# Kernel tuning notes

Hardware: AMD Instinct MI355X
Metric: run time of the kernel (lower is better)

The kernel has to match this reference:

```python
import jax, jax.numpy as jnp
import numpy as np

N = 50000      # nodes
E = 800000     # edges (avg degree 16)
IN = 128       # input feature dim
HID = 32       # per-head hidden dim
OUT = 64       # per-head output dim
H = 2          # heads per layer
NEG = 0.2      # leaky relu negative slope


def setup_inputs() -> dict:
    key = jax.random.key(0)
    ks = jax.random.split(key, 16)
    x = jax.random.normal(ks[0], (N, IN), dtype=jnp.float32)
    src = jax.random.randint(ks[1], (E,), 0, N)
    dst = jax.random.randint(ks[2], (E,), 0, N)

    def lin(k, fin, fout):
        return jax.random.normal(k, (fin, fout), dtype=jnp.float32) * (1.0 / np.sqrt(fin))

    def attn(k, h, d):
        return jax.random.normal(k, (h, d), dtype=jnp.float32) * 0.1

    # layer 0: IN -> H*HID, layer 1: H*HID -> H*HID, layer 2 (output): H*HID -> H*OUT
    W0, al0, ar0, b0 = lin(ks[3], IN, H * HID), attn(ks[4], H, HID), attn(ks[5], H, HID), jnp.zeros((H * HID,), jnp.float32)
    W1, al1, ar1, b1 = lin(ks[6], H * HID, H * HID), attn(ks[7], H, HID), attn(ks[8], H, HID), jnp.zeros((H * HID,), jnp.float32)
    W2, al2, ar2, b2 = lin(ks[9], H * HID, H * OUT), attn(ks[10], H, OUT), attn(ks[11], H, OUT), jnp.zeros((H * OUT,), jnp.float32)
    return {"x": x, "src": src, "dst": dst,
            "W0": W0, "al0": al0, "ar0": ar0, "b0": b0,
            "W1": W1, "al1": al1, "ar1": ar1, "b1": b1,
            "W2": W2, "al2": al2, "ar2": ar2, "b2": b2}


def gat_conv(x, src, dst, W, al, ar, b, heads, out_dim, apply_relu):
    # feat: [N, H, D]
    feat = (x @ W).reshape(-1, heads, out_dim)
    el = jnp.einsum('nhd,hd->nh', feat, al)   # [N, H]
    er = jnp.einsum('nhd,hd->nh', feat, ar)   # [N, H]
    # per-edge attention logits, leaky-relu
    e = jax.nn.leaky_relu(el[src] + er[dst], NEG)          # [E, H]
    # edge softmax over incoming edges of each dst node (numerically stable)
    m = jax.ops.segment_max(e, dst, num_segments=N)        # [N, H]
    m = jnp.where(jnp.isfinite(m), m, 0.0)                 # nodes w/o in-edges
    ex = jnp.exp(e - m[dst])                               # [E, H]
    s = jax.ops.segment_sum(ex, dst, num_segments=N)       # [N, H]
    alpha = ex / s[dst]                                    # [E, H]
    # weighted aggregate of source features into dst nodes
    rst = jax.ops.segment_sum(feat[src] * alpha[:, :, None], dst, num_segments=N)  # [N, H, D]
    rst = rst + b.reshape(1, heads, out_dim)
    if apply_relu:
        rst = jax.nn.relu(rst)
    return rst


def reference(x, src, dst, W0, al0, ar0, b0, W1, al1, ar1, b1, W2, al2, ar2, b2):
    h = gat_conv(x, src, dst, W0, al0, ar0, b0, H, HID, True).reshape(N, H * HID)   # flatten(1)
    h = gat_conv(h, src, dst, W1, al1, ar1, b1, H, HID, True).reshape(N, H * HID)   # flatten(1)
    logits = gat_conv(h, src, dst, W2, al2, ar2, b2, H, OUT, False).mean(axis=1)    # mean over heads -> [N, OUT]
    return logits
```

## Files before the change

kernel.cpp:

```cpp
#include <hip/hip_runtime.h>
#include <hip/hip_bf16.h>
#include <hip/hip_fp16.h>

#define NNODES 50000
#define NEG_SLOPE 0.2f
#define BKT_SHIFT 8
#define NBKT ((NNODES + 255) >> 8)
#define PEPT 8

typedef _Float16 half8 __attribute__((ext_vector_type(8)));
typedef float v4f __attribute__((ext_vector_type(4)));

__device__ __forceinline__ int rfl(int v) { return __builtin_amdgcn_readfirstlane(v); }

__device__ __forceinline__ void pack_one(const float* W, _Float16* Wp, int K, int C, int tid) {
    int KC = K / 32;
    int l = tid & 63;
    int kc = (tid >> 6) % KC;
    int t = tid / (KC * 64);
    int cc = l & 15, q = l >> 4;
    half8 b;
#pragma unroll
    for (int j = 0; j < 8; j++)
        b[j] = (_Float16)W[(size_t)(kc * 32 + q * 8 + j) * C + t * 16 + cc];
    *(half8*)(Wp + (size_t)tid * 8) = b;
}

__global__ void bucket_hist_pack(const int* __restrict__ dst, int* __restrict__ bhist, int E,
                                 const float* __restrict__ W0, _Float16* __restrict__ Wp0,
                                 const float* __restrict__ W1, _Float16* __restrict__ Wp1,
                                 const float* __restrict__ W2, _Float16* __restrict__ Wp2) {
    if (blockIdx.x >= 512) {
        int tid = (blockIdx.x - 512) * 256 + threadIdx.x;
        const int t0 = 4 * 4 * 64, t1 = 4 * 2 * 64, t2 = 8 * 2 * 64;
        if (tid < t0) pack_one(W0, Wp0, 128, 64, tid);
        else if (tid < t0 + t1) pack_one(W1, Wp1, 64, 64, tid - t0);
        else if (tid < t0 + t1 + t2) pack_one(W2, Wp2, 64, 128, tid - t0 - t1);
        return;
    }
    __shared__ int lh[NBKT];
    for (int i = threadIdx.x; i < NBKT; i += 256) lh[i] = 0;
    __syncthreads();
    const int4* d4 = (const int4*)dst;
    int E4 = E >> 2;
    for (int i = blockIdx.x * 256 + threadIdx.x; i < E4; i += 512 * 256) {
        int4 d = d4[i];
        atomicAdd(&lh[d.x >> BKT_SHIFT], 1);
        atomicAdd(&lh[d.y >> BKT_SHIFT], 1);
        atomicAdd(&lh[d.z >> BKT_SHIFT], 1);
        atomicAdd(&lh[d.w >> BKT_SHIFT], 1);
    }
    if (blockIdx.x == 0 && threadIdx.x < (E & 3))
        atomicAdd(&lh[dst[(E4 << 2) + threadIdx.x] >> BKT_SHIFT], 1);
    __syncthreads();
    for (int i = threadIdx.x; i < NBKT; i += 256)
        if (lh[i]) atomicAdd(&bhist[i], lh[i]);
}

__global__ void scan_buckets(const int* __restrict__ bhist, int* __restrict__ bbase,
                             int* __restrict__ bcursor) {
    __shared__ int buf[256];
    int t = threadIdx.x;
    int v = (t < NBKT) ? bhist[t] : 0;
    buf[t] = v;
    __syncthreads();
    for (int off = 1; off < 256; off <<= 1) {
        int x = (t >= off) ? buf[t - off] : 0;
        __syncthreads();
        buf[t] += x;
        __syncthreads();
    }
    if (t < NBKT) { int e = buf[t] - v; bbase[t] = e; bcursor[t * 16] = e; }
}

__global__ __launch_bounds__(1024) void partition_edges(
    const int* __restrict__ src, const int* __restrict__ dst,
    int* __restrict__ bcursor, int2* __restrict__ ebuf, int E) {
    __shared__ int hist[NBKT];
    __shared__ int gbase[NBKT];
    int t = threadIdx.x;
    for (int i = t; i < NBKT; i += 1024) hist[i] = 0;
    __syncthreads();
    int base = blockIdx.x * 1024 * PEPT;
    int sreg[PEPT], dreg[PEPT], rreg[PEPT], breg[PEPT];
#pragma unroll
    for (int k = 0; k < PEPT; k++) {
        int i = base + k * 1024 + t;
        if (i < E) {
            sreg[k] = src[i];
            dreg[k] = dst[i];
            breg[k] = dreg[k] >> BKT_SHIFT;
            rreg[k] = atomicAdd(&hist[breg[k]], 1);
        } else {
            breg[k] = -1;
        }
    }
    __syncthreads();
    for (int i = t; i < NBKT; i += 1024)
        if (hist[i]) gbase[i] = atomicAdd(&bcursor[i * 16], hist[i]);
    __syncthreads();
#pragma unroll
    for (int k = 0; k < PEPT; k++) {
        if (breg[k] >= 0)
            ebuf[(size_t)(gbase[breg[k]] + rreg[k])] = make_int2(sreg[k], dreg[k]);
    }
}

__global__ __launch_bounds__(256) void local_sort(const int2* __restrict__ ebuf,
                                                  const int* __restrict__ bbase,
                                                  int* __restrict__ rowptr,
                                                  int* __restrict__ csrc, int N, int E) {
    __shared__ int lcnt[256], lrow[256], ws[4];
    int b = blockIdx.x;
    int d0 = b << BKT_SHIFT;
    int t = threadIdx.x;
    int base = bbase[b];
    int endE = (b + 1 < NBKT) ? bbase[b + 1] : E;
    lcnt[t] = 0;
    __syncthreads();
    for (int i = base + t; i < endE; i += 256)
        atomicAdd(&lcnt[ebuf[i].y - d0], 1);
    __syncthreads();
    int v = lcnt[t];
    int lane = t & 63;
    int x = v;
#pragma unroll
    for (int m = 1; m < 64; m <<= 1) {
        int y = __shfl_up(x, m, 64);
        if (lane >= m) x += y;
    }
    if (lane == 63) ws[t >> 6] = x;
    __syncthreads();
    int w = t >> 6, waveoff = 0;
#pragma unroll
    for (int k = 0; k < 4; k++) if (k < w) waveoff += ws[k];
    int excl = base + waveoff + x - v;
    lrow[t] = excl;
    int d = d0 + t;
    if (d < N) rowptr[d] = excl;
    if (d == N) rowptr[N] = excl;
    lcnt[t] = 0;
    __syncthreads();
    for (int i = base + t; i < endE; i += 256) {
        int2 e = ebuf[i];
        int ld = e.y - d0;
        int p = lrow[ld] + atomicAdd(&lcnt[ld], 1);
        csrc[p] = e.x;
    }
}

template <int K, int C, bool INTERLEAVE, bool AFP32>
__global__ __launch_bounds__(256) void gemm_mfma(
    const void* __restrict__ Ahi_, const void* __restrict__ Alo_,
    const _Float16* __restrict__ Wp,
    const float* __restrict__ AL, const float* __restrict__ AR,
    void* __restrict__ featout, float2* __restrict__ el2, float2* __restrict__ er2,
    int N) {
    constexpr int KC = K / 32;
    constexpr int NT = C / 16;
    int wave = threadIdx.x >> 6, lane = threadIdx.x & 63;
    int mtile = blockIdx.x * 4 + wave;
    if (mtile * 16 >= N) return;
    int m0 = mtile * 16;
    int c = lane & 15, q = lane >> 4;

    v4f acc[NT];
#pragma unroll
    for (int t = 0; t < NT; t++) acc[t] = (v4f){0.f, 0.f, 0.f, 0.f};

    const size_t arow = (size_t)(m0 + c) * K + q * 8;
#pragma unroll
    for (int kc = 0; kc < KC; kc++) {
        half8 ah, av;
        if constexpr (AFP32) {
            const float* xr = (const float*)Ahi_ + arow + kc * 32;
            float4 f0 = *(const float4*)xr;
            float4 f1 = *(const float4*)(xr + 4);
            float fv[8] = {f0.x, f0.y, f0.z, f0.w, f1.x, f1.y, f1.z, f1.w};
#pragma unroll
            for (int j = 0; j < 8; j++) {
                ah[j] = (_Float16)fv[j];
                av[j] = (_Float16)(fv[j] - (float)ah[j]);
            }
        } else {
            ah = *(const half8*)((const _Float16*)Ahi_ + arow + kc * 32);
            av = *(const half8*)((const _Float16*)Alo_ + arow + kc * 32);
        }
#pragma unroll
        for (int t = 0; t < NT; t++) {
            half8 b = *(const half8*)(Wp + ((size_t)(t * KC + kc) * 64 + lane) * 8);
            acc[t] = __builtin_amdgcn_mfma_f32_16x16x32_f16(ah, b, acc[t], 0, 0, 0);
            acc[t] = __builtin_amdgcn_mfma_f32_16x16x32_f16(av, b, acc[t], 0, 0, 0);
        }
    }

    if (!INTERLEAVE) {
        _Float16* f16 = (_Float16*)featout;
#pragma unroll
        for (int t = 0; t < NT; t++)
#pragma unroll
            for (int r = 0; r < 4; r++) {
                int row = m0 + q * 4 + r;
                f16[(size_t)row * C + t * 16 + c] = (_Float16)acc[t][r];
            }
    } else {
        __half2* f2 = (__half2*)featout;
#pragma unroll
        for (int t = 0; t < NT / 2; t++)
#pragma unroll
            for (int r = 0; r < 4; r++) {
                int row = m0 + q * 4 + r;
                f2[(size_t)row * (C / 2) + t * 16 + c] =
                    __floats2half2_rn(acc[t][r], acc[t + NT / 2][r]);
            }
    }

    float alv[NT], arv[NT];
#pragma unroll
    for (int t = 0; t < NT; t++) { alv[t] = AL[t * 16 + c]; arv[t] = AR[t * 16 + c]; }
#pragma unroll
    for (int r = 0; r < 4; r++) {
        float l0 = 0.f, l1 = 0.f, r0 = 0.f, r1 = 0.f;
#pragma unroll
        for (int t = 0; t < NT; t++) {
            float v = acc[t][r];
            if (t < NT / 2) { l0 = fmaf(v, alv[t], l0); r0 = fmaf(v, arv[t], r0); }
            else            { l1 = fmaf(v, alv[t], l1); r1 = fmaf(v, arv[t], r1); }
        }
#pragma unroll
        for (int m = 1; m < 16; m <<= 1) {
            l0 += __shfl_xor(l0, m, 64);
            l1 += __shfl_xor(l1, m, 64);
            r0 += __shfl_xor(r0, m, 64);
            r1 += __shfl_xor(r1, m, 64);
        }
        if (c == 0) {
            int row = m0 + q * 4 + r;
            el2[row] = make_float2(l0, l1);
            er2[row] = make_float2(r0, r1);
        }
    }
}

__global__ __launch_bounds__(256) void aggregate32(
    const int* __restrict__ rowptr, const int* __restrict__ csrc,
    const float2* __restrict__ el2, const float2* __restrict__ er2,
    const _Float16* __restrict__ feat16, const float* __restrict__ b,
    _Float16* __restrict__ ahi, _Float16* __restrict__ alo, int N) {
    __shared__ int2 stA[4][64], stB[4][64];
    int wave = threadIdx.x >> 6, lane = threadIdx.x & 63, h = lane >> 5;
    int n = rfl(blockIdx.x * 4 + wave);
    if (n >= N) return;
    float bl = b[lane];
    int beg = rfl(rowptr[n]), end = rfl(rowptr[n + 1]);
    float2 rr = er2[n];
    const int2* stH = h ? stB[wave] : stA[wave];
    float s = 0.f, acc = 0.f;
    for (int base = beg; base < end; base += 64) {
        int idx = base + lane;
        int sv = 0; float wxv = 0.f, wyv = 0.f;
        if (idx < end) {
            sv = csrc[idx];
            float2 l = el2[sv];
            float t0 = l.x + rr.x; t0 = t0 > 0.f ? t0 : NEG_SLOPE * t0;
            float t1 = l.y + rr.y; t1 = t1 > 0.f ? t1 : NEG_SLOPE * t1;
            wxv = __expf(t0); wyv = __expf(t1);
        }
        stA[wave][lane] = make_int2(sv, __float_as_int(wxv));
        stB[wave][lane] = make_int2(sv, __float_as_int(wyv));
        int cnt = min(64, end - base);
        int j = 0;
        for (; j + 7 < cnt; j += 8) {
            int4 e01 = *(const int4*)(stH + j);
            int4 e23 = *(const int4*)(stH + j + 2);
            int4 e45 = *(const int4*)(stH + j + 4);
            int4 e67 = *(const int4*)(stH + j + 6);
            float f0 = (float)feat16[(size_t)e01.x * 64 + lane];
            float f1 = (float)feat16[(size_t)e01.z * 64 + lane];
            float f2 = (float)feat16[(size_t)e23.x * 64 + lane];
            float f3 = (float)feat16[(size_t)e23.z * 64 + lane];
            float f4 = (float)feat16[(size_t)e45.x * 64 + lane];
            float f5 = (float)feat16[(size_t)e45.z * 64 + lane];
            float f6 = (float)feat16[(size_t)e67.x * 64 + lane];
            float f7 = (float)feat16[(size_t)e67.z * 64 + lane];
            float w0 = __int_as_float(e01.y), w1 = __int_as_float(e01.w);
            float w2 = __int_as_float(e23.y), w3 = __int_as_float(e23.w);
            float w4 = __int_as_float(e45.y), w5 = __int_as_float(e45.w);
            float w6 = __int_as_float(e67.y), w7 = __int_as_float(e67.w);
            s += ((w0 + w1) + (w2 + w3)) + ((w4 + w5) + (w6 + w7));
            acc = fmaf(w0, f0, acc);
            acc = fmaf(w1, f1, acc);
            acc = fmaf(w2, f2, acc);
            acc = fmaf(w3, f3, acc);
            acc = fmaf(w4, f4, acc);
            acc = fmaf(w5, f5, acc);
            acc = fmaf(w6, f6, acc);
            acc = fmaf(w7, f7, acc);
        }
        for (; j < cnt; j++) {
            int2 e = stH[j];
            float w0 = __int_as_float(e.y);
            float f0 = (float)feat16[(size_t)e.x * 64 + lane];
            s += w0;
            acc = fmaf(w0, f0, acc);
        }
    }
    float v = (s > 0.f) ? acc / s : 0.f;
    v = fmaxf(v + bl, 0.f);
    _Float16 hv = (_Float16)v;
    ahi[(size_t)n * 64 + lane] = hv;
    alo[(size_t)n * 64 + lane] = (_Float16)(v - (float)hv);
}

__global__ __launch_bounds__(256) void aggregate64_mean(
    const int* __restrict__ rowptr, const int* __restrict__ csrc,
    const float2* __restrict__ el2, const float2* __restrict__ er2,
    const __half2* __restrict__ feat2, const float* __restrict__ b,
    float* __restrict__ out, int N) {
    __shared__ int4 st[4][64];
    int wave = threadIdx.x >> 6, lane = threadIdx.x & 63;
    int n = rfl(blockIdx.x * 4 + wave);
    if (n >= N) return;
    float b0 = b[lane], b1 = b[64 + lane];
    int beg = rfl(rowptr[n]), end = rfl(rowptr[n + 1]);
    float2 rr = er2[n];
    float s0 = 0.f, s1 = 0.f, a0 = 0.f, a1 = 0.f;
    for (int base = beg; base < end; base += 64) {
        int idx = base + lane;
        int sv = 0; float wxv = 0.f, wyv = 0.f;
        if (idx < end) {
            sv = csrc[idx];
            float2 l = el2[sv];
            float t0 = l.x + rr.x; t0 = t0 > 0.f ? t0 : NEG_SLOPE * t0;
            float t1 = l.y + rr.y; t1 = t1 > 0.f ? t1 : NEG_SLOPE * t1;
            wxv = __expf(t0); wyv = __expf(t1);
        }
        st[wave][lane] = make_int4(sv, __float_as_int(wxv), __float_as_int(wyv), 0);
        int cnt = min(64, end - base);
        int j = 0;
        for (; j + 7 < cnt; j += 8) {
            float2 fv[8]; float wxs[8], wys[8];
#pragma unroll
            for (int u = 0; u < 8; u++) {
                int4 e = st[wave][j + u];
                wxs[u] = __int_as_float(e.y);
                wys[u] = __int_as_float(e.z);
                fv[u] = __half22float2(feat2[(size_t)e.x * 64 + lane]);
            }
#pragma unroll
            for (int u = 0; u < 8; u++) {
                s0 += wxs[u]; s1 += wys[u];
                a0 = fmaf(wxs[u], fv[u].x, a0);
                a1 = fmaf(wys[u], fv[u].y, a1);
            }
        }
        for (; j < cnt; j++) {
            int4 e = st[wave][j];
            float wx0 = __int_as_float(e.y), wy0 = __int_as_float(e.z);
            float2 f0 = __half22float2(feat2[(size_t)e.x * 64 + lane]);
            s0 += wx0; s1 += wy0;
            a0 = fmaf(wx0, f0.x, a0); a1 = fmaf(wy0, f0.y, a1);
        }
    }
    float v0 = (s0 > 0.f) ? a0 / s0 : 0.f;
    float v1 = (s1 > 0.f) ? a1 / s1 : 0.f;
    out[(size_t)n * 64 + lane] = 0.5f * ((v0 + b0) + (v1 + b1));
}


extern "C" void kernel_launch(void* const* d_in, const int* in_sizes, int n_in,
                              void* d_out, int out_size, void* d_ws, size_t ws_size,
                              hipStream_t stream) {
    const float* x   = (const float*)d_in[0];
    const int*   src = (const int*)d_in[1];
    const int*   dst = (const int*)d_in[2];
    const float* W0  = (const float*)d_in[3];
    const float* al0 = (const float*)d_in[4];
    const float* ar0 = (const float*)d_in[5];
    const float* b0  = (const float*)d_in[6];
    const float* W1  = (const float*)d_in[7];
    const float* al1 = (const float*)d_in[8];
    const float* ar1 = (const float*)d_in[9];
    const float* b1  = (const float*)d_in[10];
    const float* W2  = (const float*)d_in[11];
    const float* al2 = (const float*)d_in[12];
    const float* ar2 = (const float*)d_in[13];
    const float* b2  = (const float*)d_in[14];
    float* out = (float*)d_out;

    const int N = NNODES;
    const int E = in_sizes[1];

    char* p = (char*)d_ws;
    auto alloc = [&](size_t bytes) {
        void* r = (void*)p;
        p += (bytes + 255) & ~(size_t)255;
        return r;
    };
    int*    bhist    = (int*)alloc((size_t)NBKT * 4);
    int*    bbase    = (int*)alloc((size_t)NBKT * 4);
    int*    bcursor  = (int*)alloc((size_t)NBKT * 16 * 4);
    int*    rowptr   = (int*)alloc((size_t)(N + 1) * 4);
    int2*   ebuf     = (int2*)alloc((size_t)E * 8);
    int*    csrc     = (int*)alloc((size_t)E * 4);
    float2* el2      = (float2*)alloc((size_t)N * 8);
    float2* er2      = (float2*)alloc((size_t)N * 8);
    _Float16* ahi    = (_Float16*)alloc((size_t)N * 64 * 2);
    _Float16* alo    = (_Float16*)alloc((size_t)N * 64 * 2);
    void*   featbuf  = alloc((size_t)N * 64 * 4);
    _Float16* Wp0    = (_Float16*)alloc(4 * 4 * 64 * 8 * 2);
    _Float16* Wp1    = (_Float16*)alloc(4 * 2 * 64 * 8 * 2);
    _Float16* Wp2    = (_Float16*)alloc(8 * 2 * 64 * 8 * 2);
    _Float16* feat16 = (_Float16*)featbuf;
    __half2*  feat2  = (__half2*)featbuf;

    hipMemsetAsync(bhist, 0, (size_t)NBKT * 4, stream);
    bucket_hist_pack<<<522, 256, 0, stream>>>(dst, bhist, E, W0, Wp0, W1, Wp1, W2, Wp2);
    scan_buckets<<<1, 256, 0, stream>>>(bhist, bbase, bcursor);
    int pb = (E + 1024 * PEPT - 1) / (1024 * PEPT);
    partition_edges<<<pb, 1024, 0, stream>>>(src, dst, bcursor, ebuf, E);
    local_sort<<<NBKT, 256, 0, stream>>>(ebuf, bbase, rowptr, csrc, N, E);

    int nb4 = (N + 3) / 4;
    int gb = (N / 16 + 3) / 4;

    gemm_mfma<128, 64, false, true><<<gb, 256, 0, stream>>>(x, nullptr, Wp0, al0, ar0, featbuf, el2, er2, N);
    aggregate32<<<nb4, 256, 0, stream>>>(rowptr, csrc, el2, er2, feat16, b0, ahi, alo, N);

    gemm_mfma<64, 64, false, false><<<gb, 256, 0, stream>>>(ahi, alo, Wp1, al1, ar1, featbuf, el2, er2, N);
    aggregate32<<<nb4, 256, 0, stream>>>(rowptr, csrc, el2, er2, feat16, b1, ahi, alo, N);

    gemm_mfma<64, 128, true, false><<<gb, 256, 0, stream>>>(ahi, alo, Wp2, al2, ar2, featbuf, el2, er2, N);
    aggregate64_mean<<<nb4, 256, 0, stream>>>(rowptr, csrc, el2, er2, feat2, b2, out, N);
}
```

Before: 257.4 us.

## Fuse all GAT stages into one persistent cooperative kernel with grid syncs

Replaces the sequence of separate launches (histogram/pack, scan, partition, local sort, three gemm and three aggregate kernels) with one cooperative persistent kernel. Each stage becomes a device phase with grid-stride loops, separated by grid.sync(), and all phases share one shared-memory union. The edge partition now walks fixed 8192-edge chunks and keeps per-edge ranks in shared memory instead of registers. This targets per-launch overhead and the memset. In exchange it adds grid-wide barrier costs, limits the grid to at most 1024 blocks, and raises shared-memory and register pressure, which may lower occupancy in the gather-heavy aggregate phases.

New measurement: 943.5 us. 267% more time.

```diff
diff --git a/kernel.cpp b/kernel.cpp
--- a/kernel.cpp
+++ b/kernel.cpp
@@ -1,17 +1,46 @@
 #include <hip/hip_runtime.h>
 #include <hip/hip_bf16.h>
 #include <hip/hip_fp16.h>
+#include <hip/hip_cooperative_groups.h>
+
+namespace cg = cooperative_groups;
 
 #define NNODES 50000
 #define NEG_SLOPE 0.2f
 #define BKT_SHIFT 8
 #define NBKT ((NNODES + 255) >> 8)
-#define PEPT 8
+#define CHUNK 8192
 
 typedef _Float16 half8 __attribute__((ext_vector_type(8)));
 typedef float v4f __attribute__((ext_vector_type(4)));
 
 __device__ __forceinline__ int rfl(int v) { return __builtin_amdgcn_readfirstlane(v); }
+
+struct PartSM { int hist[NBKT]; int gbase[NBKT]; unsigned short rank[CHUNK]; };
+struct LsortSM { int lcnt[256]; int lrow[256]; int ws[4]; };
+struct Agg32SM { int2 stA[4][64]; int2 stB[4][64]; };
+union SMem {
+    int lh[NBKT];
+    int scanbuf[256];
+    PartSM part;
+    LsortSM lsort;
+    Agg32SM agg32;
+    int4 st64[4][64];
+};
+
+struct GArgs {
+    const float* x; const int* src; const int* dst;
+    const float *W0, *al0, *ar0, *b0;
+    const float *W1, *al1, *ar1, *b1;
+    const float *W2, *al2, *ar2, *b2;
+    float* out; int E;
+    int *bhist, *bbase, *bcursor, *rowptr;
+    int2* ebuf; int* csrc;
+    float2 *el2, *er2;
+    _Float16 *ahi, *alo;
+    void* featbuf;
+    _Float16 *Wp0, *Wp1, *Wp2;
+};
 
 __device__ __forceinline__ void pack_one(const float* W, _Float16* Wp, int K, int C, int tid) {
     int KC = K / 32;
@@ -26,368 +55,350 @@
     *(half8*)(Wp + (size_t)tid * 8) = b;
 }
 
-__global__ void bucket_hist_pack(const int* __restrict__ dst, int* __restrict__ bhist, int E,
-                                 const float* __restrict__ W0, _Float16* __restrict__ Wp0,
-                                 const float* __restrict__ W1, _Float16* __restrict__ Wp1,
-                                 const float* __restrict__ W2, _Float16* __restrict__ Wp2) {
-    if (blockIdx.x >= 512) {
-        int tid = (blockIdx.x - 512) * 256 + threadIdx.x;
-        const int t0 = 4 * 4 * 64, t1 = 4 * 2 * 64, t2 = 8 * 2 * 64;
-        if (tid < t0) pack_one(W0, Wp0, 128, 64, tid);
-        else if (tid < t0 + t1) pack_one(W1, Wp1, 64, 64, tid - t0);
-        else if (tid < t0 + t1 + t2) pack_one(W2, Wp2, 64, 128, tid - t0 - t1);
-        return;
-    }
-    __shared__ int lh[NBKT];
-    for (int i = threadIdx.x; i < NBKT; i += 256) lh[i] = 0;
-    __syncthreads();
-    const int4* d4 = (const int4*)dst;
-    int E4 = E >> 2;
-    for (int i = blockIdx.x * 256 + threadIdx.x; i < E4; i += 512 * 256) {
-        int4 d = d4[i];
-        atomicAdd(&lh[d.x >> BKT_SHIFT], 1);
-        atomicAdd(&lh[d.y >> BKT_SHIFT], 1);
-        atomicAdd(&lh[d.z >> BKT_SHIFT], 1);
-        atomicAdd(&lh[d.w >> BKT_SHIFT], 1);
-    }
-    if (blockIdx.x == 0 && threadIdx.x < (E & 3))
-        atomicAdd(&lh[dst[(E4 << 2) + threadIdx.x] >> BKT_SHIFT], 1);
-    __syncthreads();
-    for (int i = threadIdx.x; i < NBKT; i += 256)
-        if (lh[i]) atomicAdd(&bhist[i], lh[i]);
-}
-
-__global__ void scan_buckets(const int* __restrict__ bhist, int* __restrict__ bbase,
-                             int* __restrict__ bcursor) {
-    __shared__ int buf[256];
-    int t = threadIdx.x;
-    int v = (t < NBKT) ? bhist[t] : 0;
-    buf[t] = v;
-    __syncthreads();
-    for (int off = 1; off < 256; off <<= 1) {
-        int x = (t >= off) ? buf[t - off] : 0;
-        __syncthreads();
-        buf[t] += x;
-        __syncthreads();
-    }
-    if (t < NBKT) { int e = buf[t] - v; bbase[t] = e; bcursor[t * 16] = e; }
-}
-
-__global__ __launch_bounds__(1024) void partition_edges(
-    const int* __restrict__ src, const int* __restrict__ dst,
-    int* __restrict__ bcursor, int2* __restrict__ ebuf, int E) {
-    __shared__ int hist[NBKT];
-    __shared__ int gbase[NBKT];
-    int t = threadIdx.x;
-    for (int i = t; i < NBKT; i += 1024) hist[i] = 0;
-    __syncthreads();
-    int base = blockIdx.x * 1024 * PEPT;
-    int sreg[PEPT], dreg[PEPT], rreg[PEPT], breg[PEPT];
-#pragma unroll
-    for (int k = 0; k < PEPT; k++) {
-        int i = base + k * 1024 + t;
-        if (i < E) {
-            sreg[k] = src[i];
-            dreg[k] = dst[i];
-            breg[k] = dreg[k] >> BKT_SHIFT;
-            rreg[k] = atomicAdd(&hist[breg[k]], 1);
-        } else {
-            breg[k] = -1;
-        }
-    }
-    __syncthreads();
-    for (int i = t; i < NBKT; i += 1024)
-        if (hist[i]) gbase[i] = atomicAdd(&bcursor[i * 16], hist[i]);
-    __syncthreads();
-#pragma unroll
-    for (int k = 0; k < PEPT; k++) {
-        if (breg[k] >= 0)
-            ebuf[(size_t)(gbase[breg[k]] + rreg[k])] = make_int2(sreg[k], dreg[k]);
-    }
-}
-
-__global__ __launch_bounds__(256) void local_sort(const int2* __restrict__ ebuf,
-                                                  const int* __restrict__ bbase,
-                                                  int* __restrict__ rowptr,
-                                                  int* __restrict__ csrc, int N, int E) {
-    __shared__ int lcnt[256], lrow[256], ws[4];
-    int b = blockIdx.x;
-    int d0 = b << BKT_SHIFT;
-    int t = threadIdx.x;
-    int base = bbase[b];
-    int endE = (b + 1 < NBKT) ? bbase[b + 1] : E;
-    lcnt[t] = 0;
-    __syncthreads();
-    for (int i = base + t; i < endE; i += 256)
-        atomicAdd(&lcnt[ebuf[i].y - d0], 1);
-    __syncthreads();
-    int v = lcnt[t];
-    int lane = t & 63;
-    int x = v;
-#pragma unroll
-    for (int m = 1; m < 64; m <<= 1) {
-        int y = __shfl_up(x, m, 64);
-        if (lane >= m) x += y;
-    }
-    if (lane == 63) ws[t >> 6] = x;
-    __syncthreads();
-    int w = t >> 6, waveoff = 0;
-#pragma unroll
-    for (int k = 0; k < 4; k++) if (k < w) waveoff += ws[k];
-    int excl = base + waveoff + x - v;
-    lrow[t] = excl;
-    int d = d0 + t;
-    if (d < N) rowptr[d] = excl;
-    if (d == N) rowptr[N] = excl;
-    lcnt[t] = 0;
-    __syncthreads();
-    for (int i = base + t; i < endE; i += 256) {
-        int2 e = ebuf[i];
-        int ld = e.y - d0;
-        int p = lrow[ld] + atomicAdd(&lcnt[ld], 1);
-        csrc[p] = e.x;
-    }
-}
-
 template <int K, int C, bool INTERLEAVE, bool AFP32>
-__global__ __launch_bounds__(256) void gemm_mfma(
-    const void* __restrict__ Ahi_, const void* __restrict__ Alo_,
-    const _Float16* __restrict__ Wp,
-    const float* __restrict__ AL, const float* __restrict__ AR,
-    void* __restrict__ featout, float2* __restrict__ el2, float2* __restrict__ er2,
-    int N) {
+__device__ void gemm_phase(const GArgs& a, const void* Ahi_, const void* Alo_,
+                           const _Float16* Wp, const float* AL, const float* AR,
+                           int gridBlocks) {
     constexpr int KC = K / 32;
     constexpr int NT = C / 16;
     int wave = threadIdx.x >> 6, lane = threadIdx.x & 63;
-    int mtile = blockIdx.x * 4 + wave;
-    if (mtile * 16 >= N) return;
-    int m0 = mtile * 16;
     int c = lane & 15, q = lane >> 4;
-
-    v4f acc[NT];
-#pragma unroll
-    for (int t = 0; t < NT; t++) acc[t] = (v4f){0.f, 0.f, 0.f, 0.f};
-
-    const size_t arow = (size_t)(m0 + c) * K + q * 8;
-#pragma unroll
-    for (int kc = 0; kc < KC; kc++) {
-        half8 ah, av;
-        if constexpr (AFP32) {
-            const float* xr = (const float*)Ahi_ + arow + kc * 32;
-            float4 f0 = *(const float4*)xr;
-            float4 f1 = *(const float4*)(xr + 4);
-            float fv[8] = {f0.x, f0.y, f0.z, f0.w, f1.x, f1.y, f1.z, f1.w};
-#pragma unroll
-            for (int j = 0; j < 8; j++) {
-                ah[j] = (_Float16)fv[j];
-                av[j] = (_Float16)(fv[j] - (float)ah[j]);
-            }
+    const int MT = NNODES / 16;
+    for (int mtile = blockIdx.x * 4 + wave; mtile < MT; mtile += gridBlocks * 4) {
+        int m0 = mtile * 16;
+        v4f acc[NT];
+#pragma unroll
+        for (int t = 0; t < NT; t++) acc[t] = (v4f){0.f, 0.f, 0.f, 0.f};
+        const size_t arow = (size_t)(m0 + c) * K + q * 8;
+#pragma unroll
+        for (int kc = 0; kc < KC; kc++) {
+            half8 ah, av;
+            if constexpr (AFP32) {
+                const float* xr = (const float*)Ahi_ + arow + kc * 32;
+                float4 f0 = *(const float4*)xr;
+                float4 f1 = *(const float4*)(xr + 4);
+                float fv[8] = {f0.x, f0.y, f0.z, f0.w, f1.x, f1.y, f1.z, f1.w};
+#pragma unroll
+                for (int j = 0; j < 8; j++) {
+                    ah[j] = (_Float16)fv[j];
+                    av[j] = (_Float16)(fv[j] - (float)ah[j]);
+                }
+            } else {
+                ah = *(const half8*)((const _Float16*)Ahi_ + arow + kc * 32);
+                av = *(const half8*)((const _Float16*)Alo_ + arow + kc * 32);
+            }
+#pragma unroll
+            for (int t = 0; t < NT; t++) {
+                half8 b = *(const half8*)(Wp + ((size_t)(t * KC + kc) * 64 + lane) * 8);
+                acc[t] = __builtin_amdgcn_mfma_f32_16x16x32_f16(ah, b, acc[t], 0, 0, 0);
+                acc[t] = __builtin_amdgcn_mfma_f32_16x16x32_f16(av, b, acc[t], 0, 0, 0);
+            }
+        }
+        if (!INTERLEAVE) {
+            _Float16* f16 = (_Float16*)a.featbuf;
+#pragma unroll
+            for (int t = 0; t < NT; t++)
+#pragma unroll
+                for (int r = 0; r < 4; r++) {
+                    int row = m0 + q * 4 + r;
+                    f16[(size_t)row * C + t * 16 + c] = (_Float16)acc[t][r];
+                }
         } else {
-            ah = *(const half8*)((const _Float16*)Ahi_ + arow + kc * 32);
-            av = *(const half8*)((const _Float16*)Alo_ + arow + kc * 32);
-        }
-#pragma unroll
-        for (int t = 0; t < NT; t++) {
-            half8 b = *(const half8*)(Wp + ((size_t)(t * KC + kc) * 64 + lane) * 8);
-            acc[t] = __builtin_amdgcn_mfma_f32_16x16x32_f16(ah, b, acc[t], 0, 0, 0);
-            acc[t] = __builtin_amdgcn_mfma_f32_16x16x32_f16(av, b, acc[t], 0, 0, 0);
-        }
-    }
-
-    if (!INTERLEAVE) {
-        _Float16* f16 = (_Float16*)featout;
-#pragma unroll
-        for (int t = 0; t < NT; t++)
-#pragma unroll
-            for (int r = 0; r < 4; r++) {
+            __half2* f2 = (__half2*)a.featbuf;
+#pragma unroll
+            for (int t = 0; t < NT / 2; t++)
+#pragma unroll
+                for (int r = 0; r < 4; r++) {
+                    int row = m0 + q * 4 + r;
+                    f2[(size_t)row * (C / 2) + t * 16 + c] =
+                        __floats2half2_rn(acc[t][r], acc[t + NT / 2][r]);
+                }
+        }
+        float alv[NT], arv[NT];
+#pragma unroll
+        for (int t = 0; t < NT; t++) { alv[t] = AL[t * 16 + c]; arv[t] = AR[t * 16 + c]; }
+#pragma unroll
+        for (int r = 0; r < 4; r++) {
+            float l0 = 0.f, l1 = 0.f, r0 = 0.f, r1 = 0.f;
+#pragma unroll
+            for (int t = 0; t < NT; t++) {
+                float v = acc[t][r];
+                if (t < NT / 2) { l0 = fmaf(v, alv[t], l0); r0 = fmaf(v, arv[t], r0); }
+                else            { l1 = fmaf(v, alv[t], l1); r1 = fmaf(v, arv[t], r1); }
+            }
+#pragma unroll
+            for (int m = 1; m < 16; m <<= 1) {
+                l0 += __shfl_xor(l0, m, 64);
+                l1 += __shfl_xor(l1, m, 64);
+                r0 += __shfl_xor(r0, m, 64);
+                r1 += __shfl_xor(r1, m, 64);
+            }
+            if (c == 0) {
                 int row = m0 + q * 4 + r;
-                f16[(size_t)row * C + t * 16 + c] = (_Float16)acc[t][r];
-            }
-    } else {
-        __half2* f2 = (__half2*)featout;
-#pragma unroll
-        for (int t = 0; t < NT / 2; t++)
-#pragma unroll
-            for (int r = 0; r < 4; r++) {
-                int row = m0 + q * 4 + r;
-                f2[(size_t)row * (C / 2) + t * 16 + c] =
-                    __floats2half2_rn(acc[t][r], acc[t + NT / 2][r]);
-            }
-    }
-
-    float alv[NT], arv[NT];
-#pragma unroll
-    for (int t = 0; t < NT; t++) { alv[t] = AL[t * 16 + c]; arv[t] = AR[t * 16 + c]; }
-#pragma unroll
-    for (int r = 0; r < 4; r++) {
-        float l0 = 0.f, l1 = 0.f, r0 = 0.f, r1 = 0.f;
-#pragma unroll
-        for (int t = 0; t < NT; t++) {
-            float v = acc[t][r];
-            if (t < NT / 2) { l0 = fmaf(v, alv[t], l0); r0 = fmaf(v, arv[t], r0); }
-            else            { l1 = fmaf(v, alv[t], l1); r1 = fmaf(v, arv[t], r1); }
-        }
-#pragma unroll
-        for (int m = 1; m < 16; m <<= 1) {
-            l0 += __shfl_xor(l0, m, 64);
-            l1 += __shfl_xor(l1, m, 64);
-            r0 += __shfl_xor(r0, m, 64);
-            r1 += __shfl_xor(r1, m, 64);
-        }
-        if (c == 0) {
-            int row = m0 + q * 4 + r;
-            el2[row] = make_float2(l0, l1);
-            er2[row] = make_float2(r0, r1);
-        }
-    }
-}
-
-__global__ __launch_bounds__(256) void aggregate32(
-    const int* __restrict__ rowptr, const int* __restrict__ csrc,
-    const float2* __restrict__ el2, const float2* __restrict__ er2,
-    const _Float16* __restrict__ feat16, const float* __restrict__ b,
-    _Float16* __restrict__ ahi, _Float16* __restrict__ alo, int N) {
-    __shared__ int2 stA[4][64], stB[4][64];
+                a.el2[row] = make_float2(l0, l1);
+                a.er2[row] = make_float2(r0, r1);
+            }
+        }
+    }
+}
+
+__device__ void agg32_phase(const GArgs& a, SMem& sm, const float* b,
+                            int gridBlocks) {
     int wave = threadIdx.x >> 6, lane = threadIdx.x & 63, h = lane >> 5;
-    int n = rfl(blockIdx.x * 4 + wave);
-    if (n >= N) return;
     float bl = b[lane];
-    int beg = rfl(rowptr[n]), end = rfl(rowptr[n + 1]);
-    float2 rr = er2[n];
-    const int2* stH = h ? stB[wave] : stA[wave];
-    float s = 0.f, acc = 0.f;
-    for (int base = beg; base < end; base += 64) {
-        int idx = base + lane;
-        int sv = 0; float wxv = 0.f, wyv = 0.f;
-        if (idx < end) {
-            sv = csrc[idx];
-            float2 l = el2[sv];
-            float t0 = l.x + rr.x; t0 = t0 > 0.f ? t0 : NEG_SLOPE * t0;
-            float t1 = l.y + rr.y; t1 = t1 > 0.f ? t1 : NEG_SLOPE * t1;
-            wxv = __expf(t0); wyv = __expf(t1);
-        }
-        stA[wave][lane] = make_int2(sv, __float_as_int(wxv));
-        stB[wave][lane] = make_int2(sv, __float_as_int(wyv));
-        int cnt = min(64, end - base);
-        int j = 0;
-        for (; j + 7 < cnt; j += 8) {
-            int4 e01 = *(const int4*)(stH + j);
-            int4 e23 = *(const int4*)(stH + j + 2);
-            int4 e45 = *(const int4*)(stH + j + 4);
-            int4 e67 = *(const int4*)(stH + j + 6);
-            float f0 = (float)feat16[(size_t)e01.x * 64 + lane];
-            float f1 = (float)feat16[(size_t)e01.z * 64 + lane];
-            float f2 = (float)feat16[(size_t)e23.x * 64 + lane];
-            float f3 = (float)feat16[(size_t)e23.z * 64 + lane];
-            float f4 = (float)feat16[(size_t)e45.x * 64 + lane];
-            float f5 = (float)feat16[(size_t)e45.z * 64 + lane];
-            float f6 = (float)feat16[(size_t)e67.x * 64 + lane];
-            float f7 = (float)feat16[(size_t)e67.z * 64 + lane];
-            float w0 = __int_as_float(e01.y), w1 = __int_as_float(e01.w);
-            float w2 = __int_as_float(e23.y), w3 = __int_as_float(e23.w);
-            float w4 = __int_as_float(e45.y), w5 = __int_as_float(e45.w);
-            float w6 = __int_as_float(e67.y), w7 = __int_as_float(e67.w);
-            s += ((w0 + w1) + (w2 + w3)) + ((w4 + w5) + (w6 + w7));
-            acc = fmaf(w0, f0, acc);
-            acc = fmaf(w1, f1, acc);
-            acc = fmaf(w2, f2, acc);
-            acc = fmaf(w3, f3, acc);
-            acc = fmaf(w4, f4, acc);
-            acc = fmaf(w5, f5, acc);
-            acc = fmaf(w6, f6, acc);
-            acc = fmaf(w7, f7, acc);
-        }
-        for (; j < cnt; j++) {
-            int2 e = stH[j];
-            float w0 = __int_as_float(e.y);
-            float f0 = (float)feat16[(size_t)e.x * 64 + lane];
-            s += w0;
-            acc = fmaf(w0, f0, acc);
-        }
-    }
-    float v = (s > 0.f) ? acc / s : 0.f;
-    v = fmaxf(v + bl, 0.f);
-    _Float16 hv = (_Float16)v;
-    ahi[(size_t)n * 64 + lane] = hv;
-    alo[(size_t)n * 64 + lane] = (_Float16)(v - (float)hv);
-}
-
-__global__ __launch_bounds__(256) void aggregate64_mean(
-    const int* __restrict__ rowptr, const int* __restrict__ csrc,
-    const float2* __restrict__ el2, const float2* __restrict__ er2,
-    const __half2* __restrict__ feat2, const float* __restrict__ b,
-    float* __restrict__ out, int N) {
-    __shared__ int4 st[4][64];
+    const _Float16* feat16 = (const _Float16*)a.featbuf;
+    const int2* stH = h ? sm.agg32.stB[wave] : sm.agg32.stA[wave];
+    for (int n0 = blockIdx.x * 4 + wave; n0 < NNODES; n0 += gridBlocks * 4) {
+        int n = rfl(n0);
+        int beg = rfl(a.rowptr[n]), end = rfl(a.rowptr[n + 1]);
+        float2 rr = a.er2[n];
+        float s = 0.f, acc = 0.f;
+        for (int base = beg; base < end; base += 64) {
+            int idx = base + lane;
+            int sv = 0; float wxv = 0.f, wyv = 0.f;
+            if (idx < end) {
+                sv = a.csrc[idx];
+                float2 l = a.el2[sv];
+                float t0 = l.x + rr.x; t0 = t0 > 0.f ? t0 : NEG_SLOPE * t0;
+                float t1 = l.y + rr.y; t1 = t1 > 0.f ? t1 : NEG_SLOPE * t1;
+                wxv = __expf(t0); wyv = __expf(t1);
+            }
+            sm.agg32.stA[wave][lane] = make_int2(sv, __float_as_int(wxv));
+            sm.agg32.stB[wave][lane] = make_int2(sv, __float_as_int(wyv));
+            int cnt = min(64, end - base);
+            int j = 0;
+            for (; j + 7 < cnt; j += 8) {
+                int4 e01 = *(const int4*)(stH + j);
+                int4 e23 = *(const int4*)(stH + j + 2);
+                int4 e45 = *(const int4*)(stH + j + 4);
+                int4 e67 = *(const int4*)(stH + j + 6);
+                float f0 = (float)feat16[(size_t)e01.x * 64 + lane];
+                float f1 = (float)feat16[(size_t)e01.z * 64 + lane];
+                float f2 = (float)feat16[(size_t)e23.x * 64 + lane];
+                float f3 = (float)feat16[(size_t)e23.z * 64 + lane];
+                float f4 = (float)feat16[(size_t)e45.x * 64 + lane];
+                float f5 = (float)feat16[(size_t)e45.z * 64 + lane];
+                float f6 = (float)feat16[(size_t)e67.x * 64 + lane];
+                float f7 = (float)feat16[(size_t)e67.z * 64 + lane];
+                float w0 = __int_as_float(e01.y), w1 = __int_as_float(e01.w);
+                float w2 = __int_as_float(e23.y), w3 = __int_as_float(e23.w);
+                float w4 = __int_as_float(e45.y), w5 = __int_as_float(e45.w);
+                float w6 = __int_as_float(e67.y), w7 = __int_as_float(e67.w);
+                s += ((w0 + w1) + (w2 + w3)) + ((w4 + w5) + (w6 + w7));
+                acc = fmaf(w0, f0, acc);
+                acc = fmaf(w1, f1, acc);
+                acc = fmaf(w2, f2, acc);
+                acc = fmaf(w3, f3, acc);
+                acc = fmaf(w4, f4, acc);
+                acc = fmaf(w5, f5, acc);
+                acc = fmaf(w6, f6, acc);
+                acc = fmaf(w7, f7, acc);
+            }
+            for (; j < cnt; j++) {
+                int2 e = stH[j];
+                float w0 = __int_as_float(e.y);
+                float f0 = (float)feat16[(size_t)e.x * 64 + lane];
+                s += w0;
+                acc = fmaf(w0, f0, acc);
+            }
+        }
+        float v = (s > 0.f) ? acc / s : 0.f;
+        v = fmaxf(v + bl, 0.f);
+        _Float16 hv = (_Float16)v;
+        a.ahi[(size_t)n * 64 + lane] = hv;
+        a.alo[(size_t)n * 64 + lane] = (_Float16)(v - (float)hv);
+    }
+}
+
+__device__ void agg64_phase(const GArgs& a, SMem& sm, const float* b,
+                            int gridBlocks) {
     int wave = threadIdx.x >> 6, lane = threadIdx.x & 63;
-    int n = rfl(blockIdx.x * 4 + wave);
-    if (n >= N) return;
     float b0 = b[lane], b1 = b[64 + lane];
-    int beg = rfl(rowptr[n]), end = rfl(rowptr[n + 1]);
-    float2 rr = er2[n];
-    float s0 = 0.f, s1 = 0.f, a0 = 0.f, a1 = 0.f;
-    for (int base = beg; base < end; base += 64) {
-        int idx = base + lane;
-        int sv = 0; float wxv = 0.f, wyv = 0.f;
-        if (idx < end) {
-            sv = csrc[idx];
-            float2 l = el2[sv];
-            float t0 = l.x + rr.x; t0 = t0 > 0.f ? t0 : NEG_SLOPE * t0;
-            float t1 = l.y + rr.y; t1 = t1 > 0.f ? t1 : NEG_SLOPE * t1;
-            wxv = __expf(t0); wyv = __expf(t1);
-        }
-        st[wave][lane] = make_int4(sv, __float_as_int(wxv), __float_as_int(wyv), 0);
-        int cnt = min(64, end - base);
-        int j = 0;
-        for (; j + 7 < cnt; j += 8) {
-            float2 fv[8]; float wxs[8], wys[8];
-#pragma unroll
-            for (int u = 0; u < 8; u++) {
-                int4 e = st[wave][j + u];
-                wxs[u] = __int_as_float(e.y);
-                wys[u] = __int_as_float(e.z);
-                fv[u] = __half22float2(feat2[(size_t)e.x * 64 + lane]);
-            }
-#pragma unroll
-            for (int u = 0; u < 8; u++) {
-                s0 += wxs[u]; s1 += wys[u];
-                a0 = fmaf(wxs[u], fv[u].x, a0);
-                a1 = fmaf(wys[u], fv[u].y, a1);
-            }
-        }
-        for (; j < cnt; j++) {
-            int4 e = st[wave][j];
-            float wx0 = __int_as_float(e.y), wy0 = __int_as_float(e.z);
-            float2 f0 = __half22float2(feat2[(size_t)e.x * 64 + lane]);
-            s0 += wx0; s1 += wy0;
-            a0 = fmaf(wx0, f0.x, a0); a1 = fmaf(wy0, f0.y, a1);
-        }
-    }
-    float v0 = (s0 > 0.f) ? a0 / s0 : 0.f;
-    float v1 = (s1 > 0.f) ? a1 / s1 : 0.f;
-    out[(size_t)n * 64 + lane] = 0.5f * ((v0 + b0) + (v1 + b1));
+    const __half2* feat2 = (const __half2*)a.featbuf;
+    for (int n0 = blockIdx.x * 4 + wave; n0 < NNODES; n0 += gridBlocks * 4) {
+        int n = rfl(n0);
+        int beg = rfl(a.rowptr[n]), end = rfl(a.rowptr[n + 1]);
+        float2 rr = a.er2[n];
+        float s0 = 0.f, s1 = 0.f, a0 = 0.f, a1 = 0.f;
+        for (int base = beg; base < end; base += 64) {
+            int idx = base + lane;
+            int sv = 0; float wxv = 0.f, wyv = 0.f;
+            if (idx < end) {
+                sv = a.csrc[idx];
+                float2 l = a.el2[sv];
+                float t0 = l.x + rr.x; t0 = t0 > 0.f ? t0 : NEG_SLOPE * t0;
+                float t1 = l.y + rr.y; t1 = t1 > 0.f ? t1 : NEG_SLOPE * t1;
+                wxv = __expf(t0); wyv = __expf(t1);
+            }
+            sm.st64[wave][lane] = make_int4(sv, __float_as_int(wxv), __float_as_int(wyv), 0);
+            int cnt = min(64, end - base);
+            int j = 0;
+            for (; j + 7 < cnt; j += 8) {
+                float2 fv[8]; float wxs[8], wys[8];
+#pragma unroll
+                for (int u = 0; u < 8; u++) {
+                    int4 e = sm.st64[wave][j + u];
+                    wxs[u] = __int_as_float(e.y);
+                    wys[u] = __int_as_float(e.z);
+                    fv[u] = __half22float2(feat2[(size_t)e.x * 64 + lane]);
+                }
+#pragma unroll
+                for (int u = 0; u < 8; u++) {
+                    s0 += wxs[u]; s1 += wys[u];
+                    a0 = fmaf(wxs[u], fv[u].x, a0);
+                    a1 = fmaf(wys[u], fv[u].y, a1);
+                }
+            }
+            for (; j < cnt; j++) {
+                int4 e = sm.st64[wave][j];
+                float wx0 = __int_as_float(e.y), wy0 = __int_as_float(e.z);
+                float2 f0 = __half22float2(feat2[(size_t)e.x * 64 + lane]);
+                s0 += wx0; s1 += wy0;
+                a0 = fmaf(wx0, f0.x, a0); a1 = fmaf(wy0, f0.y, a1);
+            }
+        }
+        float v0 = (s0 > 0.f) ? a0 / s0 : 0.f;
+        float v1 = (s1 > 0.f) ? a1 / s1 : 0.f;
+        a.out[(size_t)n * 64 + lane] = 0.5f * ((v0 + b0) + (v1 + b1));
+    }
+}
+
+__global__ __launch_bounds__(256, 4) void mega(GArgs a) {
+    __shared__ SMem sm;
+    cg::grid_group grid = cg::this_grid();
+    const int G = gridDim.x;
+    const int t = threadIdx.x;
+    const int gtid = blockIdx.x * 256 + t;
+    const int E = a.E;
+
+    if (gtid < NBKT) a.bhist[gtid] = 0;
+    {
+        const int t0 = 4 * 4 * 64, t1 = 4 * 2 * 64, t2 = 8 * 2 * 64;
+        if (gtid < t0) pack_one(a.W0, a.Wp0, 128, 64, gtid);
+        else if (gtid < t0 + t1) pack_one(a.W1, a.Wp1, 64, 64, gtid - t0);
+        else if (gtid < t0 + t1 + t2) pack_one(a.W2, a.Wp2, 64, 128, gtid - t0 - t1);
+    }
+    grid.sync();
+
+    for (int i = t; i < NBKT; i += 256) sm.lh[i] = 0;
+    __syncthreads();
+    {
+        const int4* d4 = (const int4*)a.dst;
+        int E4 = E >> 2;
+        for (int i = gtid; i < E4; i += G * 256) {
+            int4 d = d4[i];
+            atomicAdd(&sm.lh[d.x >> BKT_SHIFT], 1);
+            atomicAdd(&sm.lh[d.y >> BKT_SHIFT], 1);
+            atomicAdd(&sm.lh[d.z >> BKT_SHIFT], 1);
+            atomicAdd(&sm.lh[d.w >> BKT_SHIFT], 1);
+        }
+        if (gtid < (E & 3))
+            atomicAdd(&a.bhist[a.dst[(E4 << 2) + gtid] >> BKT_SHIFT], 1);
+    }
+    __syncthreads();
+    for (int i = t; i < NBKT; i += 256)
+        if (sm.lh[i]) atomicAdd(&a.bhist[i], sm.lh[i]);
+    grid.sync();
+
+    if (blockIdx.x == 0) {
+        int v = (t < NBKT) ? a.bhist[t] : 0;
+        sm.scanbuf[t] = v;
+        __syncthreads();
+        for (int off = 1; off < 256; off <<= 1) {
+            int x = (t >= off) ? sm.scanbuf[t - off] : 0;
+            __syncthreads();
+            sm.scanbuf[t] += x;
+            __syncthreads();
+        }
+        if (t < NBKT) { int e = sm.scanbuf[t] - v; a.bbase[t] = e; a.bcursor[t * 16] = e; }
+    }
+    grid.sync();
+
+    {
+        int nch = (E + CHUNK - 1) / CHUNK;
+        for (int ch = blockIdx.x; ch < nch; ch += G) {
+            int cbeg = ch * CHUNK, cend = min(cbeg + CHUNK, E);
+            for (int i = t; i < NBKT; i += 256) sm.part.hist[i] = 0;
+            __syncthreads();
+            for (int i = cbeg + t; i < cend; i += 256) {
+                int bkt = a.dst[i] >> BKT_SHIFT;
+                sm.part.rank[i - cbeg] = (unsigned short)atomicAdd(&sm.part.hist[bkt], 1);
+            }
+            __syncthreads();
+            for (int i = t; i < NBKT; i += 256)
+                if (sm.part.hist[i]) sm.part.gbase[i] = atomicAdd(&a.bcursor[i * 16], sm.part.hist[i]);
+            __syncthreads();
+            for (int i = cbeg + t; i < cend; i += 256) {
+                int d = a.dst[i];
+                int bkt = d >> BKT_SHIFT;
+                a.ebuf[(size_t)(sm.part.gbase[bkt] + sm.part.rank[i - cbeg])] =
+                    make_int2(a.src[i], d);
+            }
+            __syncthreads();
+        }
+    }
+    grid.sync();
+
+    {
+        for (int b = blockIdx.x; b < NBKT; b += G) {
+            int d0 = b << BKT_SHIFT;
+            int base = a.bbase[b];
+            int endE = (b + 1 < NBKT) ? a.bbase[b + 1] : E;
+            sm.lsort.lcnt[t] = 0;
+            __syncthreads();
+            for (int i = base + t; i < endE; i += 256)
+                atomicAdd(&sm.lsort.lcnt[a.ebuf[i].y - d0], 1);
+            __syncthreads();
+            int v = sm.lsort.lcnt[t];
+            int lane = t & 63;
+            int x = v;
+#pragma unroll
+            for (int m = 1; m < 64; m <<= 1) {
+                int y = __shfl_up(x, m, 64);
+                if (lane >= m) x += y;
+            }
+            if (lane == 63) sm.lsort.ws[t >> 6] = x;
+            __syncthreads();
+            int w = t >> 6, waveoff = 0;
+#pragma unroll
+            for (int k = 0; k < 4; k++) if (k < w) waveoff += sm.lsort.ws[k];
+            int excl = base + waveoff + x - v;
+            sm.lsort.lrow[t] = excl;
+            int d = d0 + t;
+            if (d < NNODES) a.rowptr[d] = excl;
+            if (d == NNODES - 1) a.rowptr[NNODES] = E;
+            sm.lsort.lcnt[t] = 0;
+            __syncthreads();
+            for (int i = base + t; i < endE; i += 256) {
+                int2 e = a.ebuf[i];
+                int ld = e.y - d0;
+                int p = sm.lsort.lrow[ld] + atomicAdd(&sm.lsort.lcnt[ld], 1);
+                a.csrc[p] = e.x;
+            }
+            __syncthreads();
+        }
+    }
+    grid.sync();
+
+    gemm_phase<128, 64, false, true>(a, a.x, nullptr, a.Wp0, a.al0, a.ar0, G);
+    grid.sync();
+    agg32_phase(a, sm, a.b0, G);
+    grid.sync();
+
+    gemm_phase<64, 64, false, false>(a, a.ahi, a.alo, a.Wp1, a.al1, a.ar1, G);
+    grid.sync();
+    agg32_phase(a, sm, a.b1, G);
+    grid.sync();
+
+    gemm_phase<64, 128, true, false>(a, a.ahi, a.alo, a.Wp2, a.al2, a.ar2, G);
+    grid.sync();
+    agg64_phase(a, sm, a.b2, G);
 }
 
 
 extern "C" void kernel_launch(void* const* d_in, const int* in_sizes, int n_in,
                               void* d_out, int out_size, void* d_ws, size_t ws_size,
                               hipStream_t stream) {
-    const float* x   = (const float*)d_in[0];
-    const int*   src = (const int*)d_in[1];
-    const int*   dst = (const int*)d_in[2];
-    const float* W0  = (const float*)d_in[3];
-    const float* al0 = (const float*)d_in[4];
-    const float* ar0 = (const float*)d_in[5];
-    const float* b0  = (const float*)d_in[6];
-    const float* W1  = (const float*)d_in[7];
-    const float* al1 = (const float*)d_in[8];
-    const float* ar1 = (const float*)d_in[9];
-    const float* b1  = (const float*)d_in[10];
-    const float* W2  = (const float*)d_in[11];
-    const float* al2 = (const float*)d_in[12];
-    const float* ar2 = (const float*)d_in[13];
-    const float* b2  = (const float*)d_in[14];
-    float* out = (float*)d_out;
-
     const int N = NNODES;
     const int E = in_sizes[1];
 
@@ -411,25 +422,34 @@
     _Float16* Wp0    = (_Float16*)alloc(4 * 4 * 64 * 8 * 2);
     _Float16* Wp1    = (_Float16*)alloc(4 * 2 * 64 * 8 * 2);
     _Float16* Wp2    = (_Float16*)alloc(8 * 2 * 64 * 8 * 2);
-    _Float16* feat16 = (_Float16*)featbuf;
-    __half2*  feat2  = (__half2*)featbuf;
-
-    hipMemsetAsync(bhist, 0, (size_t)NBKT * 4, stream);
-    bucket_hist_pack<<<522, 256, 0, stream>>>(dst, bhist, E, W0, Wp0, W1, Wp1, W2, Wp2);
-    scan_buckets<<<1, 256, 0, stream>>>(bhist, bbase, bcursor);
-    int pb = (E + 1024 * PEPT - 1) / (1024 * PEPT);
-    partition_edges<<<pb, 1024, 0, stream>>>(src, dst, bcursor, ebuf, E);
-    local_sort<<<NBKT, 256, 0, stream>>>(ebuf, bbase, rowptr, csrc, N, E);
-
-    int nb4 = (N + 3) / 4;
-    int gb = (N / 16 + 3) / 4;
-
-    gemm_mfma<128, 64, false, true><<<gb, 256, 0, stream>>>(x, nullptr, Wp0, al0, ar0, featbuf, el2, er2, N);
-    aggregate32<<<nb4, 256, 0, stream>>>(rowptr, csrc, el2, er2, feat16, b0, ahi, alo, N);
-
-    gemm_mfma<64, 64, false, false><<<gb, 256, 0, stream>>>(ahi, alo, Wp1, al1, ar1, featbuf, el2, er2, N);
-    aggregate32<<<nb4, 256, 0, stream>>>(rowptr, csrc, el2, er2, feat16, b1, ahi, alo, N);
-
-    gemm_mfma<64, 128, true, false><<<gb, 256, 0, stream>>>(ahi, alo, Wp2, al2, ar2, featbuf, el2, er2, N);
-    aggregate64_mean<<<nb4, 256, 0, stream>>>(rowptr, csrc, el2, er2, feat2, b2, out, N);
-}
+
+    GArgs a;
+    a.x   = (const float*)d_in[0];
+    a.src = (const int*)d_in[1];
+    a.dst = (const int*)d_in[2];
+    a.W0  = (const float*)d_in[3];  a.al0 = (const float*)d_in[4];
+    a.ar0 = (const float*)d_in[5];  a.b0  = (const float*)d_in[6];
+    a.W1  = (const float*)d_in[7];  a.al1 = (const float*)d_in[8];
+    a.ar1 = (const float*)d_in[9];  a.b1  = (const float*)d_in[10];
+    a.W2  = (const float*)d_in[11]; a.al2 = (const float*)d_in[12];
+    a.ar2 = (const float*)d_in[13]; a.b2  = (const float*)d_in[14];
+    a.out = (float*)d_out;
+    a.E = E;
+    a.bhist = bhist; a.bbase = bbase; a.bcursor = bcursor; a.rowptr = rowptr;
+    a.ebuf = ebuf; a.csrc = csrc; a.el2 = el2; a.er2 = er2;
+    a.ahi = ahi; a.alo = alo; a.featbuf = featbuf;
+    a.Wp0 = Wp0; a.Wp1 = Wp1; a.Wp2 = Wp2;
+
+    int dev = 0;
+    hipGetDevice(&dev);
+    int numCU = 256;
+    hipDeviceGetAttribute(&numCU, hipDeviceAttributeMultiprocessorCount, dev);
+    int maxBlk = 4;
+    hipOccupancyMaxActiveBlocksPerMultiprocessor(&maxBlk, (const void*)mega, 256, 0);
+    int G = maxBlk * numCU;
+    if (G > 1024) G = 1024;
+    if (G < 256) G = 256;
+
+    void* params[] = { (void*)&a };
+    hipLaunchCooperativeKernel((const void*)mega, dim3(G), dim3(256), params, 0, stream);
+}
```
